# Performance work log

Hardware: AMD Instinct MI355X
Metric: run time of the kernel (lower is better)

Reference implementation:

```python
import jax, jax.numpy as jnp
import numpy as np

B, S, D_IN, D_OUT = 8, 2048, 1024, 1024

def setup_inputs() -> dict:
    key = jax.random.key(0)
    k1, k2, k3, k4 = jax.random.split(key, 4)
    sc = 0.02
    return {
        "x": jax.random.normal(k1, (B, S, D_IN), dtype=jnp.float32),
        "Wq": jax.random.normal(k2, (D_IN, D_OUT), dtype=jnp.float32) * sc,
        "Wk": jax.random.normal(k3, (D_IN, D_OUT), dtype=jnp.float32) * sc,
        "Wv": jax.random.normal(k4, (D_IN, D_OUT), dtype=jnp.float32) * sc,
    }

def reference(x, Wq, Wk, Wv):
    b, n, _ = x.shape
    d_out = Wq.shape[1]
    q = jnp.einsum('bsd,de->bse', x, Wq)   # [b, n, d_out]
    k = jnp.einsum('bsd,de->bse', x, Wk)
    v = jnp.einsum('bsd,de->bse', x, Wv)
    scores = jnp.einsum('bie,bje->bij', q, k)  # [b, n, n]
    # causal mask: positions j > i set to -inf (triu, diagonal=1)
    causal = jnp.triu(jnp.ones((n, n), dtype=bool), k=1)
    scores = jnp.where(causal[None, :, :], -jnp.inf, scores)
    # NOTE: source applies softmax over dim=1 (query axis), scaled by sqrt(d_out)
    weights = jax.nn.softmax(scores / jnp.sqrt(jnp.float32(d_out)), axis=1)
    # dropout is identity in eval mode (p=0)
    return jnp.einsum('bij,bje->bie', weights, v)
```

## Files before the change

### kernel.cpp

```cpp
#include <hip/hip_runtime.h>
#include <hip/hip_bf16.h>


using bf16 = __hip_bfloat16;
typedef __attribute__((ext_vector_type(8))) short short8;
typedef __attribute__((ext_vector_type(4))) float f32x4;

__global__ void cvt_kernel(const float* __restrict__ in, bf16* __restrict__ out) {
  size_t i = ((size_t)blockIdx.x * 256 + threadIdx.x) * 4;
  float4 v = *(const float4*)(in + i);
  alignas(8) bf16 h[4] = {__float2bfloat16(v.x), __float2bfloat16(v.y),
                          __float2bfloat16(v.z), __float2bfloat16(v.w)};
  *(unsigned long long*)(out + i) = *(const unsigned long long*)h;
}

__global__ void wt_kernel(const float* __restrict__ W0, const float* __restrict__ W1,
                          const float* __restrict__ W2, bf16* __restrict__ Wt) {
  const float* W = blockIdx.z == 0 ? W0 : blockIdx.z == 1 ? W1 : W2;
  bf16* O = Wt + (size_t)blockIdx.z * 1048576ull;
  __shared__ float t[64][65];
  int n0 = blockIdx.x * 64, k0 = blockIdx.y * 64;
  int tid = threadIdx.x;
  for (int i = tid; i < 4096; i += 256) {
    int r = i >> 6, c = i & 63;
    t[r][c] = W[(size_t)(k0 + r) * 1024 + n0 + c];
  }
  __syncthreads();
  for (int i = tid; i < 4096; i += 256) {
    int r = i >> 6, c = i & 63;
    O[(size_t)(n0 + r) * 1024 + k0 + c] = __float2bfloat16(t[c][r]);
  }
}

__global__ void zero_kernel(float* p) { p[blockIdx.x * 256 + threadIdx.x] = 0.f; }

__global__ void vhat_kernel(const bf16* __restrict__ QKV, const float* __restrict__ l,
                            bf16* __restrict__ Vt) {
  int lb = blockIdx.z;
  const bf16* V = QKV + ((size_t)lb * 3 + 2) * 2097152ull;
  bf16* O = Vt + (size_t)lb * 2097152ull;
  const float* lc = l + lb * 2048;
  __shared__ float t[64][65];
  __shared__ float rl[64];
  int j0 = blockIdx.x * 64, e0 = blockIdx.y * 64;
  int tid = threadIdx.x;
  if (tid < 64) rl[tid] = 1.0f / lc[j0 + tid];
  for (int i = tid; i < 4096; i += 256) {
    int r = i >> 6, c = i & 63;
    t[r][c] = __bfloat162float(V[(size_t)(j0 + r) * 1024 + e0 + c]);
  }
  __syncthreads();
  for (int i = tid; i < 4096; i += 256) {
    int r = i >> 6, c = i & 63;
    O[(size_t)(e0 + r) * 2048 + j0 + c] = __float2bfloat16(t[c][r] * rl[c]);
  }
}

template <int EPI, bool VARK>
__global__ __launch_bounds__(256, 4) void gemm_bt(
    const bf16* __restrict__ A, const bf16* __restrict__ B, void* __restrict__ Cv,
    int lda, int ldb, int ldc, int Kin, int zdivA, int zmodB,
    unsigned long long sA, unsigned long long sB, unsigned long long sC,
    float* __restrict__ lptr) {
  if constexpr (EPI == 1) {
    if (blockIdx.x > blockIdx.y) return;
  }
  const int z = blockIdx.z;
  A += (unsigned long long)(z / zdivA) * sA;
  B += (unsigned long long)(z % zmodB) * sB;
  const int K = VARK ? (int)(blockIdx.y + 1) * 128 : Kin;

  alignas(16) __shared__ bf16 As[128 * 64];
  alignas(16) __shared__ bf16 Bs[128 * 64];

  const int tid = threadIdx.x, wave = tid >> 6, lane = tid & 63;
  const int m0 = blockIdx.y * 128, n0 = blockIdx.x * 128;
  const int srow = tid >> 3;
  const int scol_g = ((tid & 7) ^ (srow & 7)) * 8;
  const int scol_l = (tid & 7) * 8;
  const int wm = (wave >> 1) * 64, wn = (wave & 1) * 64;
  const int fm = lane & 15, sw = lane & 7, kg = lane >> 4;

  f32x4 acc[4][4];
#pragma unroll
  for (int mi = 0; mi < 4; ++mi)
#pragma unroll
    for (int ni = 0; ni < 4; ++ni) acc[mi][ni] = (f32x4){0.f, 0.f, 0.f, 0.f};

  const bf16* Arow = A + (size_t)m0 * lda;
  const bf16* Brow = B + (size_t)n0 * ldb;

  for (int k0 = 0; k0 < K; k0 += 64) {
    __syncthreads();
#pragma unroll
    for (int c = 0; c < 4; ++c) {
      int row = c * 32 + srow;
      __builtin_amdgcn_global_load_lds(
          (const __attribute__((address_space(1))) void*)(Arow + (size_t)row * lda + k0 + scol_g),
          (__attribute__((address_space(3))) void*)(As + row * 64 + scol_l), 16, 0, 0);
    }
#pragma unroll
    for (int c = 0; c < 4; ++c) {
      int row = c * 32 + srow;
      __builtin_amdgcn_global_load_lds(
          (const __attribute__((address_space(1))) void*)(Brow + (size_t)row * ldb + k0 + scol_g),
          (__attribute__((address_space(3))) void*)(Bs + row * 64 + scol_l), 16, 0, 0);
    }
    __syncthreads();
#pragma unroll
    for (int ks = 0; ks < 2; ++ks) {
      const int pc = ((ks * 4 + kg) ^ sw) * 8;
      short8 af[4], bf_[4];
#pragma unroll
      for (int i = 0; i < 4; ++i) {
        af[i] = *(const short8*)(As + (wm + i * 16 + fm) * 64 + pc);
        bf_[i] = *(const short8*)(Bs + (wn + i * 16 + fm) * 64 + pc);
      }
#pragma unroll
      for (int mi = 0; mi < 4; ++mi)
#pragma unroll
        for (int ni = 0; ni < 4; ++ni)
          acc[mi][ni] = __builtin_amdgcn_mfma_f32_16x16x32_bf16(af[mi], bf_[ni], acc[mi][ni], 0, 0, 0);
    }
  }

  const int cr = kg * 4, cc = fm;
  if constexpr (EPI == 2) {
    float* C = (float*)Cv + (unsigned long long)z * sC;
#pragma unroll
    for (int mi = 0; mi < 4; ++mi)
#pragma unroll
      for (int ni = 0; ni < 4; ++ni)
#pragma unroll
        for (int r = 0; r < 4; ++r)
          C[(size_t)(m0 + wm + mi * 16 + cr + r) * ldc + (n0 + wn + ni * 16 + cc)] = acc[mi][ni][r];
  } else if constexpr (EPI == 0) {
    bf16* C = (bf16*)Cv + (unsigned long long)z * sC;
#pragma unroll
    for (int mi = 0; mi < 4; ++mi)
#pragma unroll
      for (int ni = 0; ni < 4; ++ni)
#pragma unroll
        for (int r = 0; r < 4; ++r)
          C[(size_t)(m0 + wm + mi * 16 + cr + r) * ldc + (n0 + wn + ni * 16 + cc)] =
              __float2bfloat16(acc[mi][ni][r]);
  } else {
    bf16* C = (bf16*)Cv + (unsigned long long)z * sC;
    float colpart[4] = {0.f, 0.f, 0.f, 0.f};
#pragma unroll
    for (int mi = 0; mi < 4; ++mi)
#pragma unroll
      for (int ni = 0; ni < 4; ++ni)
#pragma unroll
        for (int r = 0; r < 4; ++r) {
          int gm = m0 + wm + mi * 16 + cr + r;
          int gn = n0 + wn + ni * 16 + cc;
          float s = acc[mi][ni][r] * 0.03125f;
          float p = (gn <= gm) ? __expf(s) : 0.f;
          colpart[ni] += p;
          C[(size_t)gm * ldc + gn] = __float2bfloat16(p);
        }
    float* lcol = lptr + (size_t)z * 2048 + n0 + wn;
#pragma unroll
    for (int ni = 0; ni < 4; ++ni) {
      float s = colpart[ni];
      s += __shfl_xor(s, 16);
      s += __shfl_xor(s, 32);
      if (lane < 16) atomicAdd(&lcol[ni * 16 + lane], s);
    }
  }
}

extern "C" void kernel_launch(void* const* d_in, const int* in_sizes, int n_in,
                              void* d_out, int out_size, void* d_ws, size_t ws_size,
                              hipStream_t stream) {
  const float* x = (const float*)d_in[0];
  const float* Wq = (const float*)d_in[1];
  const float* Wk = (const float*)d_in[2];
  const float* Wv = (const float*)d_in[3];
  float* out = (float*)d_out;

  constexpr unsigned long long X_EL = 2048ull * 1024;
  constexpr unsigned long long QKV_EL = 3ull * X_EL;
  constexpr unsigned long long P_EL = 2048ull * 2048;
  constexpr unsigned long long VT_EL = 1024ull * 2048;
  constexpr unsigned long long WT_B = 3ull * 1024 * 1024 * 2;
  constexpr unsigned long long PER_B = 2 * (X_EL + QKV_EL + P_EL + VT_EL) + 2048 * 4;

  size_t NB = 1;
  for (size_t nb : {(size_t)8, (size_t)4, (size_t)2})
    if (WT_B + nb * PER_B <= ws_size) { NB = nb; break; }

  char* p = (char*)d_ws;
  bf16* Wt = (bf16*)p;  p += WT_B;
  bf16* Xb = (bf16*)p;  p += 2 * NB * X_EL;
  bf16* QKV = (bf16*)p; p += 2 * NB * QKV_EL;
  bf16* P = (bf16*)p;   p += 2 * NB * P_EL;
  bf16* Vt = (bf16*)p;  p += 2 * NB * VT_EL;
  float* lbuf = (float*)p;

  wt_kernel<<<dim3(16, 16, 3), 256, 0, stream>>>(Wq, Wk, Wv, Wt);

  for (size_t b0 = 0; b0 < 8; b0 += NB) {
    cvt_kernel<<<dim3((unsigned)(NB * 2048)), 256, 0, stream>>>(x + b0 * X_EL, Xb);
    gemm_bt<0, false><<<dim3(8, 16, (unsigned)(NB * 3)), 256, 0, stream>>>(
        Xb, Wt, QKV, 1024, 1024, 1024, 1024, 3, 3, X_EL, 1048576ull, X_EL, nullptr);
    zero_kernel<<<dim3((unsigned)(NB * 8)), 256, 0, stream>>>(lbuf);
    gemm_bt<1, false><<<dim3(16, 16, (unsigned)NB), 256, 0, stream>>>(
        QKV, QKV + X_EL, P, 1024, 1024, 2048, 1024, 1, 1 << 30, QKV_EL, QKV_EL, P_EL, lbuf);
    vhat_kernel<<<dim3(32, 16, (unsigned)NB), 256, 0, stream>>>(QKV, lbuf, Vt);
    gemm_bt<2, true><<<dim3(8, 16, (unsigned)NB), 256, 0, stream>>>(
        P, Vt, out + b0 * X_EL, 2048, 2048, 1024, 0, 1, 1 << 30, P_EL, VT_EL, X_EL, nullptr);
  }
}
```

Before: 395.8 us.

## Remap GEMM blocks across XCDs, longest-first scheduling, vectorize transposes, fold zeroing

The GEMM kernel remaps linear block IDs round-robin across eight groups (XCD-aware placement) and, for the variable-K PV GEMM, schedules the longest-K row tiles first to cut tail imbalance. Launch bounds rise from 4 to 5 waves per SIMD. The weight and V transpose kernels switch to vectorized float4/ushort4 loads and 8-byte stores. The separate zero kernel is folded into the weight-transpose launch, with one lbuf allocated for all batches. The higher occupancy target may force register spills in the 64-accumulator GEMM.

```diff
diff --git a/kernel.cpp b/kernel.cpp
--- a/kernel.cpp
+++ b/kernel.cpp
@@ -5,6 +5,10 @@
 using bf16 = __hip_bfloat16;
 typedef __attribute__((ext_vector_type(8))) short short8;
 typedef __attribute__((ext_vector_type(4))) float f32x4;
+
+__device__ __forceinline__ float bfbits2f(unsigned short u) {
+  return __uint_as_float((unsigned)u << 16);
+}
 
 __global__ void cvt_kernel(const float* __restrict__ in, bf16* __restrict__ out) {
   size_t i = ((size_t)blockIdx.x * 256 + threadIdx.x) * 4;
@@ -15,29 +19,41 @@
 }
 
 __global__ void wt_kernel(const float* __restrict__ W0, const float* __restrict__ W1,
-                          const float* __restrict__ W2, bf16* __restrict__ Wt) {
+                          const float* __restrict__ W2, bf16* __restrict__ Wt,
+                          float* __restrict__ lbuf) {
+  int tid = threadIdx.x;
+  if (blockIdx.z == 3) {
+    int bid = blockIdx.y * 16 + blockIdx.x;
+    if (bid < 64) lbuf[bid * 256 + tid] = 0.f;
+    return;
+  }
   const float* W = blockIdx.z == 0 ? W0 : blockIdx.z == 1 ? W1 : W2;
   bf16* O = Wt + (size_t)blockIdx.z * 1048576ull;
   __shared__ float t[64][65];
   int n0 = blockIdx.x * 64, k0 = blockIdx.y * 64;
-  int tid = threadIdx.x;
-  for (int i = tid; i < 4096; i += 256) {
-    int r = i >> 6, c = i & 63;
-    t[r][c] = W[(size_t)(k0 + r) * 1024 + n0 + c];
+#pragma unroll
+  for (int i = 0; i < 4; ++i) {
+    int idx = i * 1024 + tid * 4;
+    int r = idx >> 6, c = idx & 63;
+    float4 v = *(const float4*)(W + (size_t)(k0 + r) * 1024 + n0 + c);
+    t[r][c] = v.x; t[r][c + 1] = v.y; t[r][c + 2] = v.z; t[r][c + 3] = v.w;
   }
   __syncthreads();
-  for (int i = tid; i < 4096; i += 256) {
-    int r = i >> 6, c = i & 63;
-    O[(size_t)(n0 + r) * 1024 + k0 + c] = __float2bfloat16(t[c][r]);
-  }
-}
-
-__global__ void zero_kernel(float* p) { p[blockIdx.x * 256 + threadIdx.x] = 0.f; }
+#pragma unroll
+  for (int i = 0; i < 4; ++i) {
+    int idx = i * 1024 + tid * 4;
+    int r = idx >> 6, c = idx & 63;
+    alignas(8) bf16 h[4] = {__float2bfloat16(t[c][r]), __float2bfloat16(t[c + 1][r]),
+                            __float2bfloat16(t[c + 2][r]), __float2bfloat16(t[c + 3][r])};
+    *(unsigned long long*)(O + (size_t)(n0 + r) * 1024 + k0 + c) = *(const unsigned long long*)h;
+  }
+}
 
 __global__ void vhat_kernel(const bf16* __restrict__ QKV, const float* __restrict__ l,
                             bf16* __restrict__ Vt) {
   int lb = blockIdx.z;
-  const bf16* V = QKV + ((size_t)lb * 3 + 2) * 2097152ull;
+  const unsigned short* V =
+      (const unsigned short*)QKV + ((size_t)lb * 3 + 2) * 2097152ull;
   bf16* O = Vt + (size_t)lb * 2097152ull;
   const float* lc = l + lb * 2048;
   __shared__ float t[64][65];
@@ -45,36 +61,55 @@
   int j0 = blockIdx.x * 64, e0 = blockIdx.y * 64;
   int tid = threadIdx.x;
   if (tid < 64) rl[tid] = 1.0f / lc[j0 + tid];
-  for (int i = tid; i < 4096; i += 256) {
-    int r = i >> 6, c = i & 63;
-    t[r][c] = __bfloat162float(V[(size_t)(j0 + r) * 1024 + e0 + c]);
+#pragma unroll
+  for (int i = 0; i < 4; ++i) {
+    int idx = i * 1024 + tid * 4;
+    int r = idx >> 6, c = idx & 63;
+    ushort4 u = *(const ushort4*)(V + (size_t)(j0 + r) * 1024 + e0 + c);
+    t[r][c] = bfbits2f(u.x); t[r][c + 1] = bfbits2f(u.y);
+    t[r][c + 2] = bfbits2f(u.z); t[r][c + 3] = bfbits2f(u.w);
   }
   __syncthreads();
-  for (int i = tid; i < 4096; i += 256) {
-    int r = i >> 6, c = i & 63;
-    O[(size_t)(e0 + r) * 2048 + j0 + c] = __float2bfloat16(t[c][r] * rl[c]);
+#pragma unroll
+  for (int i = 0; i < 4; ++i) {
+    int idx = i * 1024 + tid * 4;
+    int r = idx >> 6, c = idx & 63;
+    alignas(8) bf16 h[4] = {
+        __float2bfloat16(t[c][r] * rl[c]), __float2bfloat16(t[c + 1][r] * rl[c + 1]),
+        __float2bfloat16(t[c + 2][r] * rl[c + 2]), __float2bfloat16(t[c + 3][r] * rl[c + 3])};
+    *(unsigned long long*)(O + (size_t)(e0 + r) * 2048 + j0 + c) = *(const unsigned long long*)h;
   }
 }
 
 template <int EPI, bool VARK>
-__global__ __launch_bounds__(256, 4) void gemm_bt(
+__global__ __launch_bounds__(256, 5) void gemm_bt(
     const bf16* __restrict__ A, const bf16* __restrict__ B, void* __restrict__ Cv,
     int lda, int ldb, int ldc, int Kin, int zdivA, int zmodB,
     unsigned long long sA, unsigned long long sB, unsigned long long sC,
     float* __restrict__ lptr) {
+  const unsigned gx = gridDim.x, gy = gridDim.y;
+  const unsigned total = gx * gy * gridDim.z;
+  unsigned id = blockIdx.x + gx * (blockIdx.y + gy * blockIdx.z);
+  unsigned lid = (id & 7) * (total >> 3) + (id >> 3);
+  const unsigned bx = lid % gx;
+  lid /= gx;
+  const unsigned by_raw = lid % gy;
+  const unsigned bz = lid / gy;
+  const unsigned by = VARK ? (gy - 1 - by_raw) : by_raw;
+
   if constexpr (EPI == 1) {
-    if (blockIdx.x > blockIdx.y) return;
-  }
-  const int z = blockIdx.z;
+    if (bx > by) return;
+  }
+  const int z = (int)bz;
   A += (unsigned long long)(z / zdivA) * sA;
   B += (unsigned long long)(z % zmodB) * sB;
-  const int K = VARK ? (int)(blockIdx.y + 1) * 128 : Kin;
+  const int K = VARK ? (int)(by + 1) * 128 : Kin;
 
   alignas(16) __shared__ bf16 As[128 * 64];
   alignas(16) __shared__ bf16 Bs[128 * 64];
 
   const int tid = threadIdx.x, wave = tid >> 6, lane = tid & 63;
-  const int m0 = blockIdx.y * 128, n0 = blockIdx.x * 128;
+  const int m0 = by * 128, n0 = bx * 128;
   const int srow = tid >> 3;
   const int scol_g = ((tid & 7) ^ (srow & 7)) * 8;
   const int scol_l = (tid & 7) * 8;
@@ -185,30 +220,31 @@
   constexpr unsigned long long P_EL = 2048ull * 2048;
   constexpr unsigned long long VT_EL = 1024ull * 2048;
   constexpr unsigned long long WT_B = 3ull * 1024 * 1024 * 2;
-  constexpr unsigned long long PER_B = 2 * (X_EL + QKV_EL + P_EL + VT_EL) + 2048 * 4;
+  constexpr unsigned long long LB_B = 8ull * 2048 * 4;
+  constexpr unsigned long long PER_B = 2 * (X_EL + QKV_EL + P_EL + VT_EL);
 
   size_t NB = 1;
   for (size_t nb : {(size_t)8, (size_t)4, (size_t)2})
-    if (WT_B + nb * PER_B <= ws_size) { NB = nb; break; }
+    if (WT_B + LB_B + nb * PER_B <= ws_size) { NB = nb; break; }
 
   char* p = (char*)d_ws;
-  bf16* Wt = (bf16*)p;  p += WT_B;
-  bf16* Xb = (bf16*)p;  p += 2 * NB * X_EL;
-  bf16* QKV = (bf16*)p; p += 2 * NB * QKV_EL;
-  bf16* P = (bf16*)p;   p += 2 * NB * P_EL;
-  bf16* Vt = (bf16*)p;  p += 2 * NB * VT_EL;
-  float* lbuf = (float*)p;
-
-  wt_kernel<<<dim3(16, 16, 3), 256, 0, stream>>>(Wq, Wk, Wv, Wt);
+  bf16* Wt = (bf16*)p;   p += WT_B;
+  float* lbuf = (float*)p; p += LB_B;
+  bf16* Xb = (bf16*)p;   p += 2 * NB * X_EL;
+  bf16* QKV = (bf16*)p;  p += 2 * NB * QKV_EL;
+  bf16* P = (bf16*)p;    p += 2 * NB * P_EL;
+  bf16* Vt = (bf16*)p;
+
+  wt_kernel<<<dim3(16, 16, 4), 256, 0, stream>>>(Wq, Wk, Wv, Wt, lbuf);
 
   for (size_t b0 = 0; b0 < 8; b0 += NB) {
     cvt_kernel<<<dim3((unsigned)(NB * 2048)), 256, 0, stream>>>(x + b0 * X_EL, Xb);
     gemm_bt<0, false><<<dim3(8, 16, (unsigned)(NB * 3)), 256, 0, stream>>>(
         Xb, Wt, QKV, 1024, 1024, 1024, 1024, 3, 3, X_EL, 1048576ull, X_EL, nullptr);
-    zero_kernel<<<dim3((unsigned)(NB * 8)), 256, 0, stream>>>(lbuf);
     gemm_bt<1, false><<<dim3(16, 16, (unsigned)NB), 256, 0, stream>>>(
-        QKV, QKV + X_EL, P, 1024, 1024, 2048, 1024, 1, 1 << 30, QKV_EL, QKV_EL, P_EL, lbuf);
-    vhat_kernel<<<dim3(32, 16, (unsigned)NB), 256, 0, stream>>>(QKV, lbuf, Vt);
+        QKV, QKV + X_EL, P, 1024, 1024, 2048, 1024, 1, 1 << 30, QKV_EL, QKV_EL, P_EL,
+        lbuf + b0 * 2048);
+    vhat_kernel<<<dim3(32, 16, (unsigned)NB), 256, 0, stream>>>(QKV, lbuf + b0 * 2048, Vt);
     gemm_bt<2, true><<<dim3(8, 16, (unsigned)NB), 256, 0, stream>>>(
         P, Vt, out + b0 * X_EL, 2048, 2048, 1024, 0, 1, 1 << 30, P_EL, VT_EL, X_EL, nullptr);
   }
```

Result: slower. 778.8 us (+96.8%).
